# Performance work log

Hardware: AMD Instinct MI355X
Metric: run time of the kernel (lower is better)

## Reference

```python
import jax, jax.numpy as jnp
import numpy as np

N, T, V, C_IN = 256, 64, 25, 3
K = 3            # k_size
C = 64           # per-kernel channels; filters = C*K = 192
F = C * K
ALPHA = 0.2      # tf.nn.leaky_relu default alpha


def setup_inputs() -> dict:
    key = jax.random.key(0)
    k1, k2, k3 = jax.random.split(key, 3)
    x = jax.random.normal(k1, (N, T, V, C_IN), jnp.float32)
    W_conv = jax.random.normal(k2, (C_IN, F), jnp.float32) * 0.1   # 1x1 conv kernel
    W_a = jax.random.normal(k3, (2 * C, 1), jnp.float32) * 0.1     # attention 1x1 conv
    return {"x": x, "W_conv": W_conv, "W_a": W_a}


def reference(x, W_conv, W_a):
    n, t, v, _ = x.shape
    # 1x1 Conv2D == per-position linear over channel dim
    hf = jnp.einsum('ntvi,if->ntvf', x, W_conv)            # (n,t,v,C*K)
    # Rearrange 'n t v (c k) -> n t v k c'
    h = hf.reshape(n, t, v, C, K).transpose(0, 1, 2, 4, 3)  # (n,t,v,K,C)
    h = h.mean(axis=1)                                      # (n,v,K,C) temporal mean
    # a(concat[h_i, h_j]) is separable: W_a = [wa1; wa2]
    # flat index p = i*v + j: h_i[p] = h[j] (tile), h_j[p] = h[i] (repeat)
    wa1 = W_a[:C, 0]
    wa2 = W_a[C:, 0]
    s1 = jnp.einsum('nvkc,c->nvk', h, wa1)  # contribution of h_i (index j)
    s2 = jnp.einsum('nvkc,c->nvk', h, wa2)  # contribution of h_j (index i)
    E = s1[:, None, :, :] + s2[:, :, None, :]   # E[n,i,j,k], shape (n,v,v,K)
    E = jnp.where(E >= 0, E, ALPHA * E)         # leaky_relu
    # faithful raw reshape [n, v*v, k, 1] -> [n, k, v, v] as in original
    Cmat = E.reshape(n, K, v, v)
    return jax.nn.softmax(Cmat, axis=-1)
```

## Files before the change

### kernel.cpp

```cpp
#include <hip/hip_runtime.h>
#include <math.h>

#define NB    256
#define TT    64
#define VV    25
#define CIN   3
#define KK    3
#define CCH   64
#define FF    192
#define LRALPHA 0.2f

#define XROW  (VV*CIN)
#define XSLAB (TT*XROW)
#define OUTN  (VV*VV*KK)
#define NGRP  (OUTN/VV)

__global__ __launch_bounds__(256) void gat_adj_kernel(
    const float* __restrict__ x,
    const float* __restrict__ Wc,
    const float* __restrict__ Wa,
    float* __restrict__ out)
{
    const int n   = blockIdx.x;
    const int tid = threadIdx.x;

    __shared__ float psum[3][XROW];
    __shared__ float xbar[XROW];
    __shared__ float u1[CIN][KK];
    __shared__ float u2[CIN][KK];
    __shared__ float s1[VV*KK];
    __shared__ float s2[VV*KK];
    __shared__ float gmax[NGRP];
    __shared__ float ginv[NGRP];

    if (tid < 3 * XROW) {
        const int c  = tid % XROW;
        const int tc = tid / XROW;
        const float* xs = x + (size_t)n * XSLAB;
        float s = 0.f;
        for (int t = tc; t < TT; t += 3)
            s += xs[t * XROW + c];
        psum[tc][c] = s;
    }
    if (tid >= 3 * XROW && tid < 3 * XROW + 18) {
        const int j     = tid - 3 * XROW;
        const int which = j / 9;
        const int r     = j % 9;
        const int i     = r / 3, k = r % 3;
        const float* wa = Wa + which * CCH;
        float s = 0.f;
        for (int c = 0; c < CCH; ++c)
            s += Wc[i * FF + c * KK + k] * wa[c];
        if (which == 0) u1[i][k] = s; else u2[i][k] = s;
    }
    __syncthreads();

    if (tid < XROW)
        xbar[tid] = (psum[0][tid] + psum[1][tid] + psum[2][tid]) * (1.0f / TT);
    __syncthreads();

    if (tid < VV * KK) {
        const int v = tid / KK, k = tid % KK;
        float a1 = 0.f, a2 = 0.f;
        #pragma unroll
        for (int i = 0; i < CIN; ++i) {
            const float xb = xbar[v * CIN + i];
            a1 += xb * u1[i][k];
            a2 += xb * u2[i][k];
        }
        s1[tid] = a1;
        s2[tid] = a2;
    }
    __syncthreads();

    if (tid < NGRP) {
        const int g = tid;
        const int A = g / 3;
        const float* s2A = &s2[A * KK];
        float mx = -1e30f;
        float ev[VV];
        #pragma unroll
        for (int m = 0; m < VV; ++m) {
            const int i = g * VV + m;
            const int B = (i / 3) % VV;
            const int k = i % 3;
            float val = s1[B * KK + k] + s2A[k];
            val = (val >= 0.f) ? val : LRALPHA * val;
            ev[m] = val;
            mx = fmaxf(mx, val);
        }
        float sum = 0.f;
        #pragma unroll
        for (int m = 0; m < VV; ++m)
            sum += __expf(ev[m] - mx);
        gmax[g] = mx;
        ginv[g] = 1.0f / sum;
    }
    __syncthreads();

    float* op = out + (size_t)n * OUTN;
    for (int i = tid; i < OUTN; i += 256) {
        const int g = i / VV;
        const int A = i / (VV * KK);
        const int B = (i / 3) % VV;
        const int k = i % 3;
        float val = s1[B * KK + k] + s2[A * KK + k];
        val = (val >= 0.f) ? val : LRALPHA * val;
        op[i] = __expf(val - gmax[g]) * ginv[g];
    }
}

extern "C" void kernel_launch(void* const* d_in, const int* in_sizes, int n_in,
                              void* d_out, int out_size, void* d_ws, size_t ws_size,
                              hipStream_t stream) {
    const float* x  = (const float*)d_in[0];
    const float* Wc = (const float*)d_in[1];
    const float* Wa = (const float*)d_in[2];
    float* out = (float*)d_out;

    gat_adj_kernel<<<NB, 256, 0, stream>>>(x, Wc, Wa, out);
}
```

Baseline: 66.65 us.

## Vectorize temporal-mean loads, drop softmax max pass, stage exps in LDS

The temporal sum now reads x with float4 loads over 16 super-rows split across three thread groups, and the separate xbar stage is folded into the s1/s2 computation. This removes one barrier and lets 25 threads finish the mean. The softmax no longer subtracts the row max: each exponential is computed once into shared memory, then row sums are taken and a final pass scales and writes. This avoids evaluating each exp twice, but it gives up numerical overflow protection, which is only safe while the scores stay small.

```diff
diff --git a/kernel.cpp b/kernel.cpp
--- a/kernel.cpp
+++ b/kernel.cpp
@@ -14,6 +14,7 @@
 #define XSLAB (TT*XROW)
 #define OUTN  (VV*VV*KK)
 #define NGRP  (OUTN/VV)
+#define NSUP  16
 
 __global__ __launch_bounds__(256) void gat_adj_kernel(
     const float* __restrict__ x,
@@ -24,90 +25,90 @@
     const int n   = blockIdx.x;
     const int tid = threadIdx.x;
 
-    __shared__ float psum[3][XROW];
-    __shared__ float xbar[XROW];
-    __shared__ float u1[CIN][KK];
-    __shared__ float u2[CIN][KK];
-    __shared__ float s1[VV*KK];
-    __shared__ float s2[VV*KK];
-    __shared__ float gmax[NGRP];
-    __shared__ float ginv[NGRP];
+    __shared__ float4 psum4[3 * 75];
+    __shared__ float  u[2][CIN][KK];
+    __shared__ float  s1[VV * KK];
+    __shared__ float  s2[VV * KK];
+    __shared__ float  pLds[OUTN];
+    __shared__ float  ginv[NGRP];
 
-    if (tid < 3 * XROW) {
-        const int c  = tid % XROW;
-        const int tc = tid / XROW;
-        const float* xs = x + (size_t)n * XSLAB;
-        float s = 0.f;
-        for (int t = tc; t < TT; t += 3)
-            s += xs[t * XROW + c];
-        psum[tc][c] = s;
+    if (tid < 3 * 75) {
+        const int q  = tid % 75;
+        const int tc = tid / 75;
+        const float4* xv = (const float4*)(x + (size_t)n * XSLAB);
+        float4 acc = make_float4(0.f, 0.f, 0.f, 0.f);
+        #pragma unroll
+        for (int s = tc; s < NSUP; s += 3) {
+            float4 v = xv[75 * s + q];
+            acc.x += v.x; acc.y += v.y; acc.z += v.z; acc.w += v.w;
+        }
+        psum4[tid] = acc;
     }
-    if (tid >= 3 * XROW && tid < 3 * XROW + 18) {
-        const int j     = tid - 3 * XROW;
+    if (tid >= 232 && tid < 232 + 18) {
+        const int j     = tid - 232;
         const int which = j / 9;
         const int r     = j % 9;
         const int i     = r / 3, k = r % 3;
         const float* wa = Wa + which * CCH;
         float s = 0.f;
+        #pragma unroll 16
         for (int c = 0; c < CCH; ++c)
             s += Wc[i * FF + c * KK + k] * wa[c];
-        if (which == 0) u1[i][k] = s; else u2[i][k] = s;
+        u[which][i][k] = s;
     }
     __syncthreads();
 
-    if (tid < XROW)
-        xbar[tid] = (psum[0][tid] + psum[1][tid] + psum[2][tid]) * (1.0f / TT);
-    __syncthreads();
-
-    if (tid < VV * KK) {
-        const int v = tid / KK, k = tid % KK;
-        float a1 = 0.f, a2 = 0.f;
+    if (tid < VV) {
+        const int v = tid;
+        const float* psumF = (const float*)psum4;
+        float xb[CIN];
         #pragma unroll
         for (int i = 0; i < CIN; ++i) {
-            const float xb = xbar[v * CIN + i];
-            a1 += xb * u1[i][k];
-            a2 += xb * u2[i][k];
+            const int c = v * CIN + i;
+            float s = 0.f;
+            #pragma unroll
+            for (int seg = 0; seg < 4; ++seg)
+                #pragma unroll
+                for (int tc = 0; tc < 3; ++tc)
+                    s += psumF[tc * 300 + seg * 75 + c];
+            xb[i] = s * (1.0f / TT);
         }
-        s1[tid] = a1;
-        s2[tid] = a2;
+        #pragma unroll
+        for (int k = 0; k < KK; ++k) {
+            float a1 = 0.f, a2 = 0.f;
+            #pragma unroll
+            for (int i = 0; i < CIN; ++i) {
+                a1 += xb[i] * u[0][i][k];
+                a2 += xb[i] * u[1][i][k];
+            }
+            s1[v * KK + k] = a1;
+            s2[v * KK + k] = a2;
+        }
     }
     __syncthreads();
 
-    if (tid < NGRP) {
-        const int g = tid;
-        const int A = g / 3;
-        const float* s2A = &s2[A * KK];
-        float mx = -1e30f;
-        float ev[VV];
-        #pragma unroll
-        for (int m = 0; m < VV; ++m) {
-            const int i = g * VV + m;
-            const int B = (i / 3) % VV;
-            const int k = i % 3;
-            float val = s1[B * KK + k] + s2A[k];
-            val = (val >= 0.f) ? val : LRALPHA * val;
-            ev[m] = val;
-            mx = fmaxf(mx, val);
-        }
-        float sum = 0.f;
-        #pragma unroll
-        for (int m = 0; m < VV; ++m)
-            sum += __expf(ev[m] - mx);
-        gmax[g] = mx;
-        ginv[g] = 1.0f / sum;
-    }
-    __syncthreads();
-
-    float* op = out + (size_t)n * OUTN;
     for (int i = tid; i < OUTN; i += 256) {
-        const int g = i / VV;
         const int A = i / (VV * KK);
         const int B = (i / 3) % VV;
         const int k = i % 3;
         float val = s1[B * KK + k] + s2[A * KK + k];
         val = (val >= 0.f) ? val : LRALPHA * val;
-        op[i] = __expf(val - gmax[g]) * ginv[g];
+        pLds[i] = __expf(val);
     }
+    __syncthreads();
+
+    if (tid < NGRP) {
+        const float* p = &pLds[tid * VV];
+        float s = 0.f;
+        #pragma unroll
+        for (int m = 0; m < VV; ++m) s += p[m];
+        ginv[tid] = 1.0f / s;
+    }
+    __syncthreads();
+
+    float* op = out + (size_t)n * OUTN;
+    for (int i = tid; i < OUTN; i += 256)
+        op[i] = pLds[i] * ginv[i / VV];
 }
 
 extern "C" void kernel_launch(void* const* d_in, const int* in_sizes, int n_in,
```

New measurement: 61.50 us. -7.7%, faster.
